# Optimization experiments

Hardware: AMD Instinct MI355X
Metric: run time of the kernel (lower is better)

## Reference

```python
import jax, jax.numpy as jnp
import numpy as np

N_NODES = 100000
N_EDGES = 3200000
B = 64            # number of graphs / RNA batch
DIM = 16          # GINE hidden dim
NFP = 33          # protein node feature dim
EMB = 128         # embedding dim
MAXLEN = 3000     # rna_global length (conv1d in_channels)
LOCLEN = 2998     # rna_local length = 3000 - log4(64) + 1
NF = 32           # n_filters
KS = 8            # conv kernel size -> 128-8+1 = 121
FC_IN = NF * 121  # 3872
BN_EPS = 1e-5


def setup_inputs() -> dict:
    key = jax.random.key(0)
    ks = jax.random.split(key, 32)
    s = 0.1
    p = {}
    # forward data args
    p['pro_x'] = jax.random.normal(ks[0], (N_NODES, NFP), jnp.float32)
    p['pro_edge_index'] = jax.random.randint(ks[1], (2, N_EDGES), 0, N_NODES, jnp.int32)
    p['pro_weight'] = jax.random.uniform(ks[2], (N_EDGES, 1), jnp.float32)
    p['pro_batch'] = jnp.sort(jax.random.randint(ks[3], (N_NODES,), 0, B, jnp.int32))
    p['rna_global'] = jax.random.randint(ks[4], (B, MAXLEN), 0, 5, jnp.int32)
    p['rna_local'] = jax.random.randint(ks[5], (B, LOCLEN), 0, 65, jnp.int32)
    # GINE layer 1 (33 -> 16)
    p['g1_w1'] = jax.random.normal(ks[6], (NFP, DIM), jnp.float32) * s
    p['g1_b1'] = jnp.zeros((DIM,), jnp.float32)
    p['g1_w2'] = jax.random.normal(ks[7], (DIM, DIM), jnp.float32) * s
    p['g1_b2'] = jnp.zeros((DIM,), jnp.float32)
    p['g1_ew'] = jax.random.normal(ks[8], (1, NFP), jnp.float32) * s  # edge Linear(1, 33)
    p['g1_eb'] = jnp.zeros((NFP,), jnp.float32)
    p['g1_eps'] = jnp.zeros((), jnp.float32)
    # GINE layers 2-5 (16 -> 16), stacked on leading axis
    p['g_w1'] = jax.random.normal(ks[9], (4, DIM, DIM), jnp.float32) * s
    p['g_b1'] = jnp.zeros((4, DIM), jnp.float32)
    p['g_w2'] = jax.random.normal(ks[10], (4, DIM, DIM), jnp.float32) * s
    p['g_b2'] = jnp.zeros((4, DIM), jnp.float32)
    p['g_ew'] = jax.random.normal(ks[11], (4, 1, DIM), jnp.float32) * s  # edge Linear(1, 16)
    p['g_eb'] = jnp.zeros((4, DIM), jnp.float32)
    p['g_eps'] = jnp.zeros((4,), jnp.float32)
    # BatchNorm1d x5
    p['bn_gamma'] = jnp.ones((5, DIM), jnp.float32)
    p['bn_beta'] = jnp.zeros((5, DIM), jnp.float32)
    # fc1_xp (16 -> 128)
    p['fc1_xp_w'] = jax.random.normal(ks[12], (DIM, EMB), jnp.float32) * s
    p['fc1_xp_b'] = jnp.zeros((EMB,), jnp.float32)
    # RNA branch
    p['emb1'] = jax.random.normal(ks[13], (5, EMB), jnp.float32)
    p['emb2'] = jax.random.normal(ks[14], (65, EMB), jnp.float32)
    p['convr1_w'] = jax.random.normal(ks[15], (NF, MAXLEN, KS), jnp.float32) * 0.01
    p['convr1_b'] = jnp.zeros((NF,), jnp.float32)
    p['convr2_w'] = jax.random.normal(ks[16], (NF, LOCLEN, KS), jnp.float32) * 0.01
    p['convr2_b'] = jnp.zeros((NF,), jnp.float32)
    p['fcxr_w'] = jax.random.normal(ks[17], (FC_IN, EMB), jnp.float32) * 0.01
    p['fcxr_b'] = jnp.zeros((EMB,), jnp.float32)
    return p


def _gine(x, src, dst, ew, w1, b1, w2, b2, ew_w, ew_b, eps):
    # GINEConv: out = MLP((1+eps)*x + sum_j relu(x_j + edge_lin(e_ij)))
    e = ew @ ew_w + ew_b                       # [E, d]
    m = jax.nn.relu(x[src] + e)                # [E, d] gather + fuse
    agg = jax.ops.segment_sum(m, dst, num_segments=N_NODES)
    h = (1.0 + eps) * x + agg
    return jax.nn.relu(h @ w1 + b1) @ w2 + b2


def _bn(x, gamma, beta):
    mu = jnp.mean(x, axis=0)
    var = jnp.var(x, axis=0)
    return (x - mu) * jax.lax.rsqrt(var + BN_EPS) * gamma + beta


def _rna_branch(tokens, emb, cw, cb, fcw, fcb):
    x = emb[tokens]                            # [B, L, 128]
    y = jax.lax.conv_general_dilated(x, cw, (1,), 'VALID',
                                     dimension_numbers=('NCH', 'OIH', 'NCH'))
    y = y + cb[None, :, None]                  # [B, 32, 121]
    return y.reshape(y.shape[0], -1) @ fcw + fcb


def reference(pro_x, pro_edge_index, pro_weight, pro_batch, rna_global, rna_local,
              g1_w1, g1_b1, g1_w2, g1_b2, g1_ew, g1_eb, g1_eps,
              g_w1, g_b1, g_w2, g_b2, g_ew, g_eb, g_eps,
              bn_gamma, bn_beta, fc1_xp_w, fc1_xp_b,
              emb1, emb2, convr1_w, convr1_b, convr2_w, convr2_b, fcxr_w, fcxr_b):
    src, dst = pro_edge_index[0], pro_edge_index[1]
    # RNA global / local branches (shared fc_xr)
    xrg = _rna_branch(rna_global, emb1, convr1_w, convr1_b, fcxr_w, fcxr_b)
    xrl = _rna_branch(rna_local, emb2, convr2_w, convr2_b, fcxr_w, fcxr_b)
    # protein GINE stack
    xp = jax.nn.relu(_gine(pro_x, src, dst, pro_weight,
                           g1_w1, g1_b1, g1_w2, g1_b2, g1_ew, g1_eb, g1_eps))
    xp = _bn(xp, bn_gamma[0], bn_beta[0])
    for i in range(4):
        xp = jax.nn.relu(_gine(xp, src, dst, pro_weight,
                               g_w1[i], g_b1[i], g_w2[i], g_b2[i],
                               g_ew[i], g_eb[i], g_eps[i]))
        xp = _bn(xp, bn_gamma[i + 1], bn_beta[i + 1])
    # global mean pool over graphs
    sums = jax.ops.segment_sum(xp, pro_batch, num_segments=B)
    cnt = jax.ops.segment_sum(jnp.ones((N_NODES, 1), xp.dtype), pro_batch, num_segments=B)
    xp = jax.nn.relu((sums / jnp.maximum(cnt, 1.0)) @ fc1_xp_w + fc1_xp_b)
    # dropout in eval mode -> identity
    xc_rna = 0.5 * (xrg + xrl)
    return (xc_rna, xp)
```

## Files before the change

### kernel.cpp

```cpp
#include <hip/hip_runtime.h>
#include <hip/hip_fp16.h>

#define N_NODES 100000
#define N_EDGES 3200000
#define BGR 64
#define DIM 16
#define NFP 33
#define ROW1 32
#define H1STR 36
#define EMB 128
#define MAXLEN 3000
#define LOCLEN 2998
#define NF 32
#define KS 8
#define OUTT 121
#define FC_IN 3872
#define BN_EPSV 1e-5f
#define POOL_CHUNK 256
#define POOL_BLKS 391
#define MLPB 391
#define AGGB1 6250
#define AGGB16 3125
#define NBIN 391
#define BCNT_BLK 512
#define P1_CHUNK 4096
#define P1_BLOCKS 782
#define MAXBIN 9088
#define NKC 32
#define KCH 121
#define WDEC (1.f / 32767.f)
#define SEG_G 8

__global__ void __launch_bounds__(256) k_bincnt(const int* __restrict__ dst,
                                                int* __restrict__ bh) {
    __shared__ int hist[NBIN];
    int t = threadIdx.x, bid = blockIdx.x;
    for (int b = t; b < NBIN; b += 256) hist[b] = 0;
    __syncthreads();
    int e0 = bid * (N_EDGES / BCNT_BLK);
    int e1 = e0 + (N_EDGES / BCNT_BLK);
    for (int e = e0 + t; e < e1; e += 256) atomicAdd(&hist[dst[e] >> 8], 1);
    __syncthreads();
    for (int b = t; b < NBIN; b += 256) bh[b * BCNT_BLK + bid] = hist[b];
}

__global__ void __launch_bounds__(512) k_binscan(const int* __restrict__ bh,
                                                 int* __restrict__ binoff,
                                                 int* __restrict__ bincur) {
    __shared__ int sc[512];
    int t = threadIdx.x;
    int s = 0;
    if (t < NBIN) {
        const int4* row = (const int4*)(bh + t * BCNT_BLK);
        #pragma unroll 4
        for (int k = 0; k < BCNT_BLK / 4; k++) {
            int4 v = row[k];
            s += v.x + v.y + v.z + v.w;
        }
    }
    sc[t] = s;
    __syncthreads();
    for (int off = 1; off < 512; off <<= 1) {
        int v = (t >= off) ? sc[t - off] : 0;
        __syncthreads();
        sc[t] += v;
        __syncthreads();
    }
    int excl = sc[t] - s;
    if (t <= NBIN) binoff[t] = excl;
    if (t < NBIN) bincur[t] = excl;
}

__global__ void __launch_bounds__(256) k_part1(const int* __restrict__ src,
                                               const int* __restrict__ dst,
                                               const float* __restrict__ w,
                                               int* __restrict__ bincur,
                                               int2* __restrict__ tmp_sw) {
    __shared__ int2 srec[P1_CHUNK];
    __shared__ unsigned short sbin[P1_CHUNK];
    __shared__ unsigned short sperm[P1_CHUNK];
    __shared__ int hist[NBIN];
    __shared__ int off[NBIN];
    __shared__ int cur[NBIN];
    __shared__ int base[NBIN];
    __shared__ int sc[512];
    int t = threadIdx.x;
    int g0 = blockIdx.x * P1_CHUNK;
    int cn = N_EDGES - g0; if (cn > P1_CHUNK) cn = P1_CHUNK;
    for (int b = t; b < NBIN; b += 256) hist[b] = 0;
    __syncthreads();
    for (int j = t; j < cn; j += 256) {
        int d = dst[g0 + j];
        int b = d >> 8;
        sbin[j] = (unsigned short)b;
        srec[j] = make_int2(src[g0 + j] | ((d & 255) << 20), __float_as_int(w[g0 + j]));
        atomicAdd(&hist[b], 1);
    }
    __syncthreads();
    sc[t] = (t < NBIN) ? hist[t] : 0;
    sc[256 + t] = (256 + t < NBIN) ? hist[256 + t] : 0;
    __syncthreads();
    for (int o = 1; o <= 256; o <<= 1) {
        int v0 = (t >= o) ? sc[t - o] : 0;
        int v1 = sc[256 + t - o];
        __syncthreads();
        sc[t] += v0;
        sc[256 + t] += v1;
        __syncthreads();
    }
    for (int b = t; b < NBIN; b += 256) {
        int e = sc[b] - hist[b];
        off[b] = e;
        cur[b] = e;
        int c = hist[b];
        base[b] = c ? atomicAdd(&bincur[b], c) : 0;
    }
    __syncthreads();
    for (int j = t; j < cn; j += 256) {
        int p = atomicAdd(&cur[sbin[j]], 1);
        sperm[p] = (unsigned short)j;
    }
    __syncthreads();
    for (int p = t; p < cn; p += 256) {
        int j = sperm[p];
        int b = sbin[j];
        tmp_sw[base[b] + (p - off[b])] = srec[j];
    }
}

__global__ void __launch_bounds__(256) k_part2(const int2* __restrict__ tmp_sw,
                                               const int* __restrict__ binoff,
                                               unsigned* __restrict__ er,
                                               int* __restrict__ ptr) {
    __shared__ unsigned char sdl[MAXBIN];
    __shared__ unsigned short perm[MAXBIN];
    __shared__ int hist[256];
    __shared__ int cur[256];
    __shared__ int sc[256];
    int t = threadIdx.x, b = blockIdx.x;
    int nlo = b << 8;
    int e0 = binoff[b], e1 = binoff[b + 1];
    int cnt = e1 - e0;
    int stage = cnt < MAXBIN ? cnt : MAXBIN;
    hist[t] = 0;
    __syncthreads();
    for (int j = t; j < stage; j += 256) {
        unsigned char dl = (unsigned char)((tmp_sw[e0 + j].x >> 20) & 255);
        sdl[j] = dl;
        atomicAdd(&hist[dl], 1);
    }
    for (int j = stage + t; j < cnt; j += 256)
        atomicAdd(&hist[(tmp_sw[e0 + j].x >> 20) & 255], 1);
    __syncthreads();
    int v = hist[t];
    sc[t] = v;
    __syncthreads();
    for (int off = 1; off < 256; off <<= 1) {
        int u = (t >= off) ? sc[t - off] : 0;
        __syncthreads();
        sc[t] += u;
        __syncthreads();
    }
    int excl = sc[t] - v;
    cur[t] = excl;
    if (nlo + t < N_NODES) ptr[nlo + t] = e0 + excl;
    if (b == NBIN - 1 && t == 0) ptr[N_NODES] = N_EDGES;
    __syncthreads();
    for (int j = t; j < stage; j += 256) {
        int p = atomicAdd(&cur[sdl[j]], 1);
        perm[p] = (unsigned short)j;
    }
    __syncthreads();
    for (int j = stage + t; j < cnt; j += 256) {
        int2 sw = tmp_sw[e0 + j];
        int p = atomicAdd(&cur[(sw.x >> 20) & 255], 1);
        unsigned wq = (unsigned)(__int_as_float(sw.y) * 32767.f + 0.5f);
        er[e0 + p] = ((unsigned)sw.x & 0x1FFFFu) | (wq << 17);
    }
    for (int p = t; p < stage; p += 256) {
        int2 sw = tmp_sw[e0 + perm[p]];
        unsigned wq = (unsigned)(__int_as_float(sw.y) * 32767.f + 0.5f);
        er[e0 + p] = ((unsigned)sw.x & 0x1FFFFu) | (wq << 17);
    }
}

__global__ void k_half1(const float* __restrict__ x, __half* __restrict__ xh,
                        __half* __restrict__ xh32) {
    int i = blockIdx.x * blockDim.x + threadIdx.x;
    if (i < N_NODES * NFP) {
        int n = i / NFP, f = i - n * NFP;
        __half v = __float2half(x[i]);
        if (f < 32) xh[n * ROW1 + f] = v;
        else xh32[n] = v;
    }
}

__global__ void __launch_bounds__(256) k_cwt(const float* __restrict__ cw,
                                             float* __restrict__ cwT, int L) {
    int l = blockIdx.x;
    int ok = threadIdx.x;
    cwT[l * 256 + ok] = cw[(ok >> 3) * (L * KS) + l * KS + (ok & 7)];
}

__device__ __forceinline__ void acc8p(float a[8], uint4 r, float wv,
                                      const float* __restrict__ ewf,
                                      const float* __restrict__ ebf) {
    float2 f01 = __half22float2(*(__half2*)&r.x);
    float2 f23 = __half22float2(*(__half2*)&r.y);
    float2 f45 = __half22float2(*(__half2*)&r.z);
    float2 f67 = __half22float2(*(__half2*)&r.w);
    float x[8] = {f01.x, f01.y, f23.x, f23.y, f45.x, f45.y, f67.x, f67.y};
    #pragma unroll
    for (int j = 0; j < 8; j++)
        a[j] += fmaxf(x[j] + fmaf(wv, ewf[j], ebf[j]), 0.f);
}

__device__ __forceinline__ void acc8s(float a[8], uint4 r, float wv,
                                      const float* __restrict__ scf,
                                      const float* __restrict__ cbf,
                                      const float* __restrict__ ewf) {
    float2 f01 = __half22float2(*(__half2*)&r.x);
    float2 f23 = __half22float2(*(__half2*)&r.y);
    float2 f45 = __half22float2(*(__half2*)&r.z);
    float2 f67 = __half22float2(*(__half2*)&r.w);
    float x[8] = {f01.x, f01.y, f23.x, f23.y, f45.x, f45.y, f67.x, f67.y};
    #pragma unroll
    for (int j = 0; j < 8; j++)
        a[j] += fmaxf(fmaf(x[j], scf[j], fmaf(wv, ewf[j], cbf[j])), 0.f);
}

__global__ void __launch_bounds__(256) k_agg1(
    const __half* __restrict__ xh, const __half* __restrict__ xh32,
    const int* __restrict__ ptr, const unsigned* __restrict__ er,
    const float* __restrict__ ew, const float* __restrict__ ebv,
    const float* __restrict__ epsp, float* __restrict__ h) {
    int t = threadIdx.x;
    int wave = t >> 6, lane = t & 63;
    int nl = lane >> 4;
    int slot = (lane >> 2) & 3;
    int q = lane & 3;
    float ewf[8], ebf[8];
    #pragma unroll
    for (int j = 0; j < 8; j++) { ewf[j] = ew[q * 8 + j]; ebf[j] = ebv[q * 8 + j]; }
    float ew32 = ew[32], eb32 = ebv[32];
    float ep = 1.f + epsp[0];
    int node = blockIdx.x * 16 + wave * 4 + nl;
    int e0 = ptr[node], e1 = ptr[node + 1];
    float a[8] = {0, 0, 0, 0, 0, 0, 0, 0};
    float a32 = 0.f;
    int i = e0 + slot;
    while (i + 4 < e1) {
        unsigned ev0 = er[i];
        unsigned ev1 = er[i + 4];
        int s0 = ev0 & 0x1FFFF, s1 = ev1 & 0x1FFFF;
        float wv0 = (float)(ev0 >> 17) * WDEC;
        float wv1 = (float)(ev1 >> 17) * WDEC;
        uint4 r0 = *(const uint4*)(xh + s0 * ROW1 + q * 8);
        uint4 r1 = *(const uint4*)(xh + s1 * ROW1 + q * 8);
        acc8p(a, r0, wv0, ewf, ebf);
        acc8p(a, r1, wv1, ewf, ebf);
        if (q == 0) {
            a32 += fmaxf(__half2float(xh32[s0]) + fmaf(wv0, ew32, eb32), 0.f);
            a32 += fmaxf(__half2float(xh32[s1]) + fmaf(wv1, ew32, eb32), 0.f);
        }
        i += 8;
    }
    if (i < e1) {
        unsigned ev = er[i];
        int s = ev & 0x1FFFF;
        float wv = (float)(ev >> 17) * WDEC;
        uint4 r = *(const uint4*)(xh + s * ROW1 + q * 8);
        acc8p(a, r, wv, ewf, ebf);
        if (q == 0)
            a32 += fmaxf(__half2float(xh32[s]) + fmaf(wv, ew32, eb32), 0.f);
    }
    #pragma unroll
    for (int j = 0; j < 8; j++) {
        a[j] += __shfl_xor(a[j], 4);
        a[j] += __shfl_xor(a[j], 8);
    }
    a32 += __shfl_xor(a32, 4);
    a32 += __shfl_xor(a32, 8);
    if (slot == 0) {
        uint4 sraw = *(const uint4*)(xh + node * ROW1 + q * 8);
        float2 s01 = __half22float2(*(__half2*)&sraw.x);
        float2 s23 = __half22float2(*(__half2*)&sraw.y);
        float2 s45 = __half22float2(*(__half2*)&sraw.z);
        float2 s67 = __half22float2(*(__half2*)&sraw.w);
        float* hp = h + node * H1STR + q * 8;
        *(float4*)hp = make_float4(ep * s01.x + a[0], ep * s01.y + a[1],
                                   ep * s23.x + a[2], ep * s23.y + a[3]);
        *(float4*)(hp + 4) = make_float4(ep * s45.x + a[4], ep * s45.y + a[5],
                                         ep * s67.x + a[6], ep * s67.y + a[7]);
        if (q == 0)
            h[node * H1STR + 32] = ep * __half2float(xh32[node]) + a32;
    }
}

__global__ void __launch_bounds__(256) k_agg16(
    const __half* __restrict__ zh, const int* __restrict__ ptr,
    const unsigned* __restrict__ er,
    const float* __restrict__ ew, const float* __restrict__ ebv,
    const float* __restrict__ epsp,
    const float* __restrict__ bnstat, const float* __restrict__ gamma,
    const float* __restrict__ beta, float* __restrict__ h) {
    int t = threadIdx.x;
    int wave = t >> 6, lane = t & 63;
    int nl = lane >> 3;
    int slot = (lane >> 1) & 3;
    int hh = lane & 1;
    float ep = 1.f + epsp[0];
    const float invn = 1.f / (float)N_NODES;
    float scf[8], shf[8], cbf[8], ewf[8];
    #pragma unroll
    for (int j = 0; j < 8; j++) {
        int f = hh * 8 + j;
        float mu = bnstat[f] * invn;
        float var = bnstat[DIM + f] * invn - mu * mu;
        float sc = gamma[f] * rsqrtf(var + BN_EPSV);
        scf[j] = sc;
        shf[j] = beta[f] - mu * sc;
        cbf[j] = shf[j] + ebv[f];
        ewf[j] = ew[f];
    }
    int node = blockIdx.x * 32 + wave * 8 + nl;
    int e0 = ptr[node], e1 = ptr[node + 1];
    float a[8] = {0, 0, 0, 0, 0, 0, 0, 0};
    int i = e0 + slot;
    while (i + 4 < e1) {
        unsigned ev0 = er[i];
        unsigned ev1 = er[i + 4];
        float wv0 = (float)(ev0 >> 17) * WDEC;
        float wv1 = (float)(ev1 >> 17) * WDEC;
        uint4 r0 = *(const uint4*)(zh + (ev0 & 0x1FFFFu) * DIM + hh * 8);
        uint4 r1 = *(const uint4*)(zh + (ev1 & 0x1FFFFu) * DIM + hh * 8);
        acc8s(a, r0, wv0, scf, cbf, ewf);
        acc8s(a, r1, wv1, scf, cbf, ewf);
        i += 8;
    }
    if (i < e1) {
        unsigned ev = er[i];
        float wv = (float)(ev >> 17) * WDEC;
        uint4 r = *(const uint4*)(zh + (ev & 0x1FFFFu) * DIM + hh * 8);
        acc8s(a, r, wv, scf, cbf, ewf);
    }
    #pragma unroll
    for (int j = 0; j < 8; j++) a[j] += __shfl_xor(a[j], 2);
    #pragma unroll
    for (int j = 0; j < 8; j++) a[j] += __shfl_xor(a[j], 4);
    if (slot == 0) {
        uint4 sraw = *(const uint4*)(zh + node * DIM + hh * 8);
        float2 s01 = __half22float2(*(__half2*)&sraw.x);
        float2 s23 = __half22float2(*(__half2*)&sraw.y);
        float2 s45 = __half22float2(*(__half2*)&sraw.z);
        float2 s67 = __half22float2(*(__half2*)&sraw.w);
        float xs[8] = {s01.x, s01.y, s23.x, s23.y, s45.x, s45.y, s67.x, s67.y};
        float o8[8];
        #pragma unroll
        for (int j = 0; j < 8; j++)
            o8[j] = ep * fmaf(xs[j], scf[j], shf[j]) + a[j];
        float* hp = h + node * DIM + hh * 8;
        *(float4*)hp = make_float4(o8[0], o8[1], o8[2], o8[3]);
        *(float4*)(hp + 4) = make_float4(o8[4], o8[5], o8[6], o8[7]);
    }
}

__device__ __forceinline__ void mlp_bn_tail(float zv[16], bool active, int t,
                                            float* __restrict__ part) {
    __shared__ float red[4][32];
    float zs[16], zq[16];
    #pragma unroll
    for (int o = 0; o < 16; o++) {
        zs[o] = active ? zv[o] : 0.f;
        zq[o] = active ? zv[o] * zv[o] : 0.f;
    }
    #pragma unroll
    for (int m = 1; m <= 32; m <<= 1) {
        #pragma unroll
        for (int o = 0; o < 16; o++) {
            zs[o] += __shfl_xor(zs[o], m);
            zq[o] += __shfl_xor(zq[o], m);
        }
    }
    int wave = t >> 6, lane = t & 63;
    if (lane == 0) {
        #pragma unroll
        for (int o = 0; o < 16; o++) {
            red[wave][o] = zs[o];
            red[wave][16 + o] = zq[o];
        }
    }
    __syncthreads();
    if (t < 32)
        part[blockIdx.x * 32 + t] = red[0][t] + red[1][t] + red[2][t] + red[3][t];
}

__device__ __forceinline__ void store_zh(__half* __restrict__ zh, int n, float zv[16]) {
    __half2 p[8];
    #pragma unroll
    for (int j = 0; j < 8; j++) p[j] = __floats2half2_rn(zv[2 * j], zv[2 * j + 1]);
    *(uint4*)(zh + n * DIM) = *(uint4*)&p[0];
    *(uint4*)(zh + n * DIM + 8) = *(uint4*)&p[4];
}

__global__ void __launch_bounds__(256) k_mlp16(
    const float* __restrict__ h,
    const float* __restrict__ W1, const float* __restrict__ b1,
    const float* __restrict__ W2, const float* __restrict__ b2,
    __half* __restrict__ zh, float* __restrict__ part) {
    __shared__ float W1s[256], W2s[256], b1s[16], b2s[16];
    int t = threadIdx.x;
    W1s[t] = W1[t];
    W2s[t] = W2[t];
    if (t < 16) { b1s[t] = b1[t]; b2s[t] = b2[t]; }
    __syncthreads();
    int n = blockIdx.x * 256 + t;
    bool active = n < N_NODES;
    float zv[16];
    if (active) {
        float hv[16];
        #pragma unroll
        for (int j = 0; j < 4; j++) {
            float4 v = *(const float4*)(h + n * DIM + j * 4);
            hv[j * 4] = v.x; hv[j * 4 + 1] = v.y; hv[j * 4 + 2] = v.z; hv[j * 4 + 3] = v.w;
        }
        float tv[16];
        #pragma unroll
        for (int o = 0; o < 16; o++) {
            float s = b1s[o];
            #pragma unroll
            for (int f = 0; f < 16; f++) s += hv[f] * W1s[f * 16 + o];
            tv[o] = fmaxf(s, 0.f);
        }
        #pragma unroll
        for (int o = 0; o < 16; o++) {
            float s = b2s[o];
            #pragma unroll
            for (int f = 0; f < 16; f++) s += tv[f] * W2s[f * 16 + o];
            zv[o] = fmaxf(s, 0.f);
        }
        store_zh(zh, n, zv);
    }
    mlp_bn_tail(zv, active, t, part);
}

__global__ void __launch_bounds__(256) k_mlp1(
    const float* __restrict__ h,
    const float* __restrict__ W1, const float* __restrict__ b1,
    const float* __restrict__ W2, const float* __restrict__ b2,
    __half* __restrict__ zh, float* __restrict__ part) {
    __shared__ float W1s[NFP * 16], W2s[256], b1s[16], b2s[16];
    int t = threadIdx.x;
    for (int j = t; j < NFP * 16; j += 256) W1s[j] = W1[j];
    W2s[t] = W2[t];
    if (t < 16) { b1s[t] = b1[t]; b2s[t] = b2[t]; }
    __syncthreads();
    int n = blockIdx.x * 256 + t;
    bool active = n < N_NODES;
    float zv[16];
    if (active) {
        float hv[NFP];
        #pragma unroll
        for (int j = 0; j < 8; j++) {
            float4 v = *(const float4*)(h + n * H1STR + j * 4);
            hv[j * 4] = v.x; hv[j * 4 + 1] = v.y; hv[j * 4 + 2] = v.z; hv[j * 4 + 3] = v.w;
        }
        hv[32] = h[n * H1STR + 32];
        float tv[16];
        #pragma unroll
        for (int o = 0; o < 16; o++) {
            float s = b1s[o];
            #pragma unroll
            for (int f = 0; f < NFP; f++) s += hv[f] * W1s[f * 16 + o];
            tv[o] = fmaxf(s, 0.f);
        }
        #pragma unroll
        for (int o = 0; o < 16; o++) {
            float s = b2s[o];
            #pragma unroll
            for (int f = 0; f < 16; f++) s += tv[f] * W2s[f * 16 + o];
            zv[o] = fmaxf(s, 0.f);
        }
        store_zh(zh, n, zv);
    }
    mlp_bn_tail(zv, active, t, part);
}

__global__ void __launch_bounds__(1024) k_bnred(const float* __restrict__ part,
                                                float* __restrict__ bnstat) {
    __shared__ float red[1024];
    int t = threadIdx.x;
    int f = t & 31, g = t >> 5;
    float s = 0.f;
    for (int i = g; i < MLPB; i += 32) s += part[i * 32 + f];
    red[t] = s;
    __syncthreads();
    for (int off = 512; off >= 32; off >>= 1) {
        if (t < off) red[t] += red[t + off];
        __syncthreads();
    }
    if (t < 32) bnstat[t] = red[t];
}

__global__ void __launch_bounds__(256) k_pool(const __half* __restrict__ zh,
                                              const int* __restrict__ batch,
                                              const float* __restrict__ bnstat,
                                              const float* __restrict__ gamma,
                                              const float* __restrict__ beta,
                                              float* __restrict__ gsum,
                                              float* __restrict__ gcnt) {
    __shared__ float lsum[BGR * DIM];
    __shared__ float lcnt[BGR];
    int t = threadIdx.x;
    for (int j = t; j < BGR * DIM; j += 256) lsum[j] = 0.f;
    if (t < BGR) lcnt[t] = 0.f;
    __syncthreads();
    int f = t & 15, r = t >> 4;
    const float invn = 1.f / (float)N_NODES;
    float mu = bnstat[f] * invn;
    float var = bnstat[DIM + f] * invn - mu * mu;
    float sc = gamma[f] * rsqrtf(var + BN_EPSV);
    float sh = beta[f] - mu * sc;
    int start = blockIdx.x * POOL_CHUNK;
    float acc = 0.f, cacc = 0.f;
    int cur = -1;
    for (int i = 0; i < POOL_CHUNK / 16; i++) {
        int n = start + r + i * 16;
        if (n >= N_NODES) break;
        int b = batch[n];
        if (b != cur) {
            if (cur >= 0) {
                atomicAdd(&lsum[cur * DIM + f], acc);
                if (f == 0) atomicAdd(&lcnt[cur], cacc);
            }
            cur = b; acc = 0.f; cacc = 0.f;
        }
        acc += fmaf(__half2float(zh[n * DIM + f]), sc, sh);
        cacc += 1.f;
    }
    if (cur >= 0) {
        atomicAdd(&lsum[cur * DIM + f], acc);
        if (f == 0) atomicAdd(&lcnt[cur], cacc);
    }
    __syncthreads();
    for (int j = t; j < BGR * DIM; j += 256) {
        float v = lsum[j];
        if (v != 0.f) atomicAdd(&gsum[j], v);
    }
    if (t < BGR) {
        float v = lcnt[t];
        if (v != 0.f) atomicAdd(&gcnt[t], v);
    }
}

__global__ void k_xp(const float* __restrict__ gsum, const float* __restrict__ gcnt,
                     const float* __restrict__ w, const float* __restrict__ bias,
                     float* __restrict__ out) {
    int b = blockIdx.x;
    int e = threadIdx.x;
    float inv = 1.f / fmaxf(gcnt[b], 1.f);
    float acc = bias[e];
    #pragma unroll
    for (int f = 0; f < DIM; f++) acc += gsum[b * DIM + f] * inv * w[f * EMB + e];
    out[b * EMB + e] = fmaxf(acc, 0.f);
}

__global__ void __launch_bounds__(256) k_bucket(const int* __restrict__ tok, int L, int V,
                                                int* __restrict__ blist,
                                                int* __restrict__ bptr) {
    __shared__ int hist[65];
    __shared__ int cursor[65];
    int b = blockIdx.x, t = threadIdx.x;
    if (t < V) hist[t] = 0;
    __syncthreads();
    for (int l = t; l < L; l += 256) atomicAdd(&hist[tok[b * L + l]], 1);
    __syncthreads();
    if (t == 0) {
        int run = 0;
        for (int v = 0; v < V; v++) {
            cursor[v] = run;
            bptr[b * (V + 1) + v] = run;
            run += hist[v];
        }
        bptr[b * (V + 1) + V] = run;
    }
    __syncthreads();
    for (int l = t; l < L; l += 256) {
        int v = tok[b * L + l];
        int p = atomicAdd(&cursor[v], 1);
        blist[b * L + p] = l;
    }
}

__global__ void __launch_bounds__(256) k_wsum_g(const int* __restrict__ blist,
                                                const int* __restrict__ bptr,
                                                const float* __restrict__ cwT,
                                                float* __restrict__ Wp) {
    int b = blockIdx.x, v = blockIdx.y, seg = blockIdx.z;
    int t = threadIdx.x;
    int s = bptr[b * 6 + v], e = bptr[b * 6 + v + 1];
    int cnt = e - s;
    int chunk = (cnt + SEG_G - 1) / SEG_G;
    int j0 = s + seg * chunk;
    int j1 = j0 + chunk; if (j1 > e) j1 = e;
    const int* bl = blist + b * MAXLEN;
    float acc = 0.f;
    int j = j0;
    while (j + 3 < j1) {
        int t0 = bl[j], t1 = bl[j + 1], t2 = bl[j + 2], t3 = bl[j + 3];
        float a0 = cwT[t0 * 256 + t];
        float a1 = cwT[t1 * 256 + t];
        float a2 = cwT[t2 * 256 + t];
        float a3 = cwT[t3 * 256 + t];
        acc += a0 + a1 + a2 + a3;
        j += 4;
    }
    while (j < j1) {
        acc += cwT[bl[j] * 256 + t];
        j++;
    }
    Wp[((b * 5 + v) * SEG_G + seg) * 256 + t] = acc;
}

__global__ void __launch_bounds__(256) k_wsum_l(const int* __restrict__ blist,
                                                const int* __restrict__ bptr,
                                                const float* __restrict__ cwT,
                                                float* __restrict__ W) {
    int b = blockIdx.x, v = blockIdx.y;
    int t = threadIdx.x;
    int s = bptr[b * 66 + v], e = bptr[b * 66 + v + 1];
    const int* bl = blist + b * LOCLEN;
    float acc = 0.f;
    int j = s;
    while (j + 3 < e) {
        int t0 = bl[j], t1 = bl[j + 1], t2 = bl[j + 2], t3 = bl[j + 3];
        float a0 = cwT[t0 * 256 + t];
        float a1 = cwT[t1 * 256 + t];
        float a2 = cwT[t2 * 256 + t];
        float a3 = cwT[t3 * 256 + t];
        acc += a0 + a1 + a2 + a3;
        j += 4;
    }
    while (j < e) {
        acc += cwT[bl[j] * 256 + t];
        j++;
    }
    int o = t >> 3, k = t & 7;
    W[((b * NF + o) * 65 + v) * KS + k] = acc;
}

__global__ void k_y(const float* __restrict__ Wpg, const float* __restrict__ Wl,
                    const float* __restrict__ emb1, const float* __restrict__ emb2,
                    const float* __restrict__ cb1, const float* __restrict__ cb2,
                    float* __restrict__ yg, float* __restrict__ yl) {
    int which = blockIdx.y;
    int bo = blockIdx.x;
    int b = bo >> 5, o = bo & 31;
    int t = threadIdx.x;
    const float* emb = which ? emb2 : emb1;
    const float* cb = which ? cb2 : cb1;
    float* y = which ? yl : yg;
    int V = which ? 65 : 5;
    __shared__ float Wsh[65 * KS];
    if (which) {
        const float* Wrow = Wl + (b * NF + o) * 65 * KS;
        for (int j = t; j < 65 * KS; j += 128) Wsh[j] = Wrow[j];
    } else {
        for (int j = t; j < 5 * KS; j += 128) {
            int v = j >> 3, k = j & 7;
            const float* p = Wpg + (b * 5 + v) * SEG_G * 256 + o * 8 + k;
            float s = 0.f;
            #pragma unroll
            for (int g = 0; g < SEG_G; g++) s += p[g * 256];
            Wsh[j] = s;
        }
    }
    __syncthreads();
    if (t < OUTT) {
        float acc = cb[o];
        for (int v = 0; v < V; v++) {
            const float* ep = emb + v * EMB + t;
            #pragma unroll
            for (int k = 0; k < KS; k++) acc += Wsh[v * KS + k] * ep[k];
        }
        y[(b * NF + o) * OUTT + t] = acc;
    }
}

__global__ void __launch_bounds__(128) k_fcpart(const float* __restrict__ yg,
                                                const float* __restrict__ yl,
                                                const float* __restrict__ w,
                                                float* __restrict__ partial) {
    int b = blockIdx.x, which = blockIdx.y, kc = blockIdx.z;
    const float* y = which ? yl : yg;
    int e = threadIdx.x;
    __shared__ float ych[KCH];
    int j0 = kc * KCH;
    if (e < KCH) ych[e] = y[b * FC_IN + j0 + e];
    __syncthreads();
    float acc = 0.f;
    #pragma unroll 4
    for (int jj = 0; jj < KCH; jj++) acc += ych[jj] * w[(j0 + jj) * EMB + e];
    partial[((which * BGR + b) * NKC + kc) * EMB + e] = acc;
}

__global__ void k_fcred(const float* __restrict__ partial, const float* __restrict__ bias,
                        float* __restrict__ out) {
    int b = blockIdx.x;
    int e = threadIdx.x;
    const float* pg = partial + b * NKC * EMB + e;
    const float* pl = partial + (BGR + b) * NKC * EMB + e;
    float ag = bias[e], al = bias[e];
    #pragma unroll
    for (int k = 0; k < NKC; k++) { ag += pg[k * EMB]; al += pl[k * EMB]; }
    out[b * EMB + e] = 0.5f * (ag + al);
}

extern "C" void kernel_launch(void* const* d_in, const int* in_sizes, int n_in,
                              void* d_out, int out_size, void* d_ws, size_t ws_size,
                              hipStream_t stream) {
    const float* pro_x = (const float*)d_in[0];
    const int* eidx = (const int*)d_in[1];
    const int* esrc = eidx;
    const int* edst = eidx + N_EDGES;
    const float* pw = (const float*)d_in[2];
    const int* batch = (const int*)d_in[3];
    const int* rg = (const int*)d_in[4];
    const int* rl = (const int*)d_in[5];
    const float* g1_w1 = (const float*)d_in[6];
    const float* g1_b1 = (const float*)d_in[7];
    const float* g1_w2 = (const float*)d_in[8];
    const float* g1_b2 = (const float*)d_in[9];
    const float* g1_ew = (const float*)d_in[10];
    const float* g1_eb = (const float*)d_in[11];
    const float* g1_eps = (const float*)d_in[12];
    const float* g_w1 = (const float*)d_in[13];
    const float* g_b1 = (const float*)d_in[14];
    const float* g_w2 = (const float*)d_in[15];
    const float* g_b2 = (const float*)d_in[16];
    const float* g_ew = (const float*)d_in[17];
    const float* g_eb = (const float*)d_in[18];
    const float* g_eps = (const float*)d_in[19];
    const float* bn_gamma = (const float*)d_in[20];
    const float* bn_beta = (const float*)d_in[21];
    const float* fc1_xp_w = (const float*)d_in[22];
    const float* fc1_xp_b = (const float*)d_in[23];
    const float* emb1 = (const float*)d_in[24];
    const float* emb2 = (const float*)d_in[25];
    const float* convr1_w = (const float*)d_in[26];
    const float* convr1_b = (const float*)d_in[27];
    const float* convr2_w = (const float*)d_in[28];
    const float* convr2_b = (const float*)d_in[29];
    const float* fcxr_w = (const float*)d_in[30];
    const float* fcxr_b = (const float*)d_in[31];
    float* out = (float*)d_out;

    float* wsf = (float*)d_ws;
    int* ptr       = (int*)wsf;        wsf += 100128;
    int* binoff    = (int*)wsf;        wsf += 512;
    int* bincur    = (int*)wsf;        wsf += 512;
    unsigned* er   = (unsigned*)wsf;   wsf += 2 * N_EDGES;
    float* stats   = wsf;              wsf += 1280;
    float* un = wsf;
    int2* tmp_sw = (int2*)un;
    int* bh      = (int*)(un + 7200000);
    float* cwTg  = un;
    float* cwTl  = un + 768000;
    __half* zh   = (__half*)(un + 1600000);
    __half* xh1  = (__half*)(un + 2400000);
    __half* xh32 = (__half*)(un + 4000000);
    float* bpart = un + 4100000;
    float* Wpg   = un + 4300000;
    float* Wl    = un + 5000000;
    float* yg    = un + 6100000;
    float* yl    = un + 6350000;
    int* blg     = (int*)(un + 6600000);
    int* bll     = (int*)(un + 6800000);
    int* bpg     = (int*)(un + 7000000);
    int* bpl     = (int*)(un + 7001000);
    float* fcpart = un + 7100000;
    float* h      = un + 7400000;
    float* gsum   = stats;
    float* gcnt   = stats + 1024;
    float* bnstat = stats + 1088;

    hipMemsetAsync(stats, 0, 1280 * sizeof(float), stream);

    k_bincnt<<<BCNT_BLK, 256, 0, stream>>>(edst, bh);
    k_binscan<<<1, 512, 0, stream>>>(bh, binoff, bincur);
    k_part1<<<P1_BLOCKS, 256, 0, stream>>>(esrc, edst, pw, bincur, tmp_sw);
    k_part2<<<NBIN, 256, 0, stream>>>(tmp_sw, binoff, er, ptr);

    k_cwt<<<MAXLEN, 256, 0, stream>>>(convr1_w, cwTg, MAXLEN);
    k_cwt<<<LOCLEN, 256, 0, stream>>>(convr2_w, cwTl, LOCLEN);

    k_half1<<<(N_NODES * NFP + 255) / 256, 256, 0, stream>>>(pro_x, xh1, xh32);

    k_bucket<<<BGR, 256, 0, stream>>>(rg, MAXLEN, 5, blg, bpg);
    k_bucket<<<BGR, 256, 0, stream>>>(rl, LOCLEN, 65, bll, bpl);
    k_wsum_g<<<dim3(BGR, 5, SEG_G), 256, 0, stream>>>(blg, bpg, cwTg, Wpg);
    k_wsum_l<<<dim3(BGR, 65), 256, 0, stream>>>(bll, bpl, cwTl, Wl);
    k_y<<<dim3(BGR * NF, 2), 128, 0, stream>>>(Wpg, Wl, emb1, emb2, convr1_b, convr2_b, yg, yl);
    k_fcpart<<<dim3(BGR, 2, NKC), 128, 0, stream>>>(yg, yl, fcxr_w, fcpart);
    k_fcred<<<BGR, 128, 0, stream>>>(fcpart, fcxr_b, out);

    k_agg1<<<AGGB1, 256, 0, stream>>>(xh1, xh32, ptr, er, g1_ew, g1_eb, g1_eps, h);
    k_mlp1<<<MLPB, 256, 0, stream>>>(h, g1_w1, g1_b1, g1_w2, g1_b2, zh, bpart);
    k_bnred<<<1, 1024, 0, stream>>>(bpart, bnstat);
    for (int i = 0; i < 4; i++) {
        k_agg16<<<AGGB16, 256, 0, stream>>>(zh, ptr, er,
                                            g_ew + i * DIM, g_eb + i * DIM, g_eps + i,
                                            bnstat + i * 32, bn_gamma + i * DIM,
                                            bn_beta + i * DIM, h);
        k_mlp16<<<MLPB, 256, 0, stream>>>(h, g_w1 + i * DIM * DIM, g_b1 + i * DIM,
                                          g_w2 + i * DIM * DIM, g_b2 + i * DIM, zh, bpart);
        k_bnred<<<1, 1024, 0, stream>>>(bpart, bnstat + (i + 1) * 32);
    }
    k_pool<<<POOL_BLKS, 256, 0, stream>>>(zh, batch, bnstat + 4 * 32,
                                          bn_gamma + 4 * DIM, bn_beta + 4 * DIM, gsum, gcnt);
    k_xp<<<BGR, EMB, 0, stream>>>(gsum, gcnt, fc1_xp_w, fc1_xp_b, out + BGR * EMB);
}
```

Measured before the change: 618.2 us.

## Merge small RNA-branch kernels and replace BN partial reduction with atomics

The paired global/local RNA kernels (weight transpose, bucketing, weighted sums) are merged into single launches indexed by block coordinate. The conv output kernel is fused with the fc partial product, so per-filter outputs stay in shared memory instead of round-tripping through global buffers. The separate one-block BatchNorm statistic reduction kernels are removed: each MLP block atomically adds its partial sums into the stats buffer, which is zeroed at the start. This cuts around a dozen launches and some global traffic, at the cost of nondeterministic float atomic summation order.

```diff
diff --git a/kernel.cpp b/kernel.cpp
--- a/kernel.cpp
+++ b/kernel.cpp
@@ -195,11 +195,18 @@
     }
 }
 
-__global__ void __launch_bounds__(256) k_cwt(const float* __restrict__ cw,
-                                             float* __restrict__ cwT, int L) {
+__global__ void __launch_bounds__(256) k_cwt2(const float* __restrict__ cw1,
+                                              const float* __restrict__ cw2,
+                                              float* __restrict__ cwTg,
+                                              float* __restrict__ cwTl) {
     int l = blockIdx.x;
     int ok = threadIdx.x;
-    cwT[l * 256 + ok] = cw[(ok >> 3) * (L * KS) + l * KS + (ok & 7)];
+    if (l < MAXLEN) {
+        cwTg[l * 256 + ok] = cw1[(ok >> 3) * (MAXLEN * KS) + l * KS + (ok & 7)];
+    } else {
+        int ll = l - MAXLEN;
+        cwTl[ll * 256 + ok] = cw2[(ok >> 3) * (LOCLEN * KS) + ll * KS + (ok & 7)];
+    }
 }
 
 __device__ __forceinline__ void acc8p(float a[8], uint4 r, float wv,
@@ -366,7 +373,7 @@
 }
 
 __device__ __forceinline__ void mlp_bn_tail(float zv[16], bool active, int t,
-                                            float* __restrict__ part) {
+                                            float* __restrict__ bnstat) {
     __shared__ float red[4][32];
     float zs[16], zq[16];
     #pragma unroll
@@ -392,7 +399,7 @@
     }
     __syncthreads();
     if (t < 32)
-        part[blockIdx.x * 32 + t] = red[0][t] + red[1][t] + red[2][t] + red[3][t];
+        atomicAdd(&bnstat[t], red[0][t] + red[1][t] + red[2][t] + red[3][t]);
 }
 
 __device__ __forceinline__ void store_zh(__half* __restrict__ zh, int n, float zv[16]) {
@@ -407,7 +414,7 @@
     const float* __restrict__ h,
     const float* __restrict__ W1, const float* __restrict__ b1,
     const float* __restrict__ W2, const float* __restrict__ b2,
-    __half* __restrict__ zh, float* __restrict__ part) {
+    __half* __restrict__ zh, float* __restrict__ bnstat) {
     __shared__ float W1s[256], W2s[256], b1s[16], b2s[16];
     int t = threadIdx.x;
     W1s[t] = W1[t];
@@ -441,14 +448,14 @@
         }
         store_zh(zh, n, zv);
     }
-    mlp_bn_tail(zv, active, t, part);
+    mlp_bn_tail(zv, active, t, bnstat);
 }
 
 __global__ void __launch_bounds__(256) k_mlp1(
     const float* __restrict__ h,
     const float* __restrict__ W1, const float* __restrict__ b1,
     const float* __restrict__ W2, const float* __restrict__ b2,
-    __half* __restrict__ zh, float* __restrict__ part) {
+    __half* __restrict__ zh, float* __restrict__ bnstat) {
     __shared__ float W1s[NFP * 16], W2s[256], b1s[16], b2s[16];
     int t = threadIdx.x;
     for (int j = t; j < NFP * 16; j += 256) W1s[j] = W1[j];
@@ -483,23 +490,7 @@
         }
         store_zh(zh, n, zv);
     }
-    mlp_bn_tail(zv, active, t, part);
-}
-
-__global__ void __launch_bounds__(1024) k_bnred(const float* __restrict__ part,
-                                                float* __restrict__ bnstat) {
-    __shared__ float red[1024];
-    int t = threadIdx.x;
-    int f = t & 31, g = t >> 5;
-    float s = 0.f;
-    for (int i = g; i < MLPB; i += 32) s += part[i * 32 + f];
-    red[t] = s;
-    __syncthreads();
-    for (int off = 512; off >= 32; off >>= 1) {
-        if (t < off) red[t] += red[t + off];
-        __syncthreads();
-    }
-    if (t < 32) bnstat[t] = red[t];
+    mlp_bn_tail(zv, active, t, bnstat);
 }
 
 __global__ void __launch_bounds__(256) k_pool(const __half* __restrict__ zh,
@@ -565,11 +556,18 @@
     out[b * EMB + e] = fmaxf(acc, 0.f);
 }
 
-__global__ void __launch_bounds__(256) k_bucket(const int* __restrict__ tok, int L, int V,
-                                                int* __restrict__ blist,
-                                                int* __restrict__ bptr) {
+__global__ void __launch_bounds__(256) k_bucket2(const int* __restrict__ tg,
+                                                 const int* __restrict__ tl,
+                                                 int* __restrict__ blg, int* __restrict__ bpg,
+                                                 int* __restrict__ bll, int* __restrict__ bpl) {
     __shared__ int hist[65];
     __shared__ int cursor[65];
+    int which = blockIdx.y;
+    const int* tok = which ? tl : tg;
+    int L = which ? LOCLEN : MAXLEN;
+    int V = which ? 65 : 5;
+    int* blist = which ? bll : blg;
+    int* bptr = which ? bpl : bpg;
     int b = blockIdx.x, t = threadIdx.x;
     if (t < V) hist[t] = 0;
     __syncthreads();
@@ -592,76 +590,81 @@
     }
 }
 
-__global__ void __launch_bounds__(256) k_wsum_g(const int* __restrict__ blist,
-                                                const int* __restrict__ bptr,
-                                                const float* __restrict__ cwT,
-                                                float* __restrict__ Wp) {
-    int b = blockIdx.x, v = blockIdx.y, seg = blockIdx.z;
+__global__ void __launch_bounds__(256) k_wsum(const int* __restrict__ blg,
+                                              const int* __restrict__ bpg,
+                                              const int* __restrict__ bll,
+                                              const int* __restrict__ bpl,
+                                              const float* __restrict__ cwTg,
+                                              const float* __restrict__ cwTl,
+                                              float* __restrict__ Wp,
+                                              float* __restrict__ Wlocal) {
+    int b = blockIdx.x, y = blockIdx.y;
     int t = threadIdx.x;
-    int s = bptr[b * 6 + v], e = bptr[b * 6 + v + 1];
-    int cnt = e - s;
-    int chunk = (cnt + SEG_G - 1) / SEG_G;
-    int j0 = s + seg * chunk;
-    int j1 = j0 + chunk; if (j1 > e) j1 = e;
-    const int* bl = blist + b * MAXLEN;
-    float acc = 0.f;
-    int j = j0;
-    while (j + 3 < j1) {
-        int t0 = bl[j], t1 = bl[j + 1], t2 = bl[j + 2], t3 = bl[j + 3];
-        float a0 = cwT[t0 * 256 + t];
-        float a1 = cwT[t1 * 256 + t];
-        float a2 = cwT[t2 * 256 + t];
-        float a3 = cwT[t3 * 256 + t];
-        acc += a0 + a1 + a2 + a3;
-        j += 4;
-    }
-    while (j < j1) {
-        acc += cwT[bl[j] * 256 + t];
-        j++;
-    }
-    Wp[((b * 5 + v) * SEG_G + seg) * 256 + t] = acc;
-}
-
-__global__ void __launch_bounds__(256) k_wsum_l(const int* __restrict__ blist,
-                                                const int* __restrict__ bptr,
-                                                const float* __restrict__ cwT,
-                                                float* __restrict__ W) {
-    int b = blockIdx.x, v = blockIdx.y;
-    int t = threadIdx.x;
-    int s = bptr[b * 66 + v], e = bptr[b * 66 + v + 1];
-    const int* bl = blist + b * LOCLEN;
-    float acc = 0.f;
-    int j = s;
-    while (j + 3 < e) {
-        int t0 = bl[j], t1 = bl[j + 1], t2 = bl[j + 2], t3 = bl[j + 3];
-        float a0 = cwT[t0 * 256 + t];
-        float a1 = cwT[t1 * 256 + t];
-        float a2 = cwT[t2 * 256 + t];
-        float a3 = cwT[t3 * 256 + t];
-        acc += a0 + a1 + a2 + a3;
-        j += 4;
-    }
-    while (j < e) {
-        acc += cwT[bl[j] * 256 + t];
-        j++;
-    }
-    int o = t >> 3, k = t & 7;
-    W[((b * NF + o) * 65 + v) * KS + k] = acc;
-}
-
-__global__ void k_y(const float* __restrict__ Wpg, const float* __restrict__ Wl,
-                    const float* __restrict__ emb1, const float* __restrict__ emb2,
-                    const float* __restrict__ cb1, const float* __restrict__ cb2,
-                    float* __restrict__ yg, float* __restrict__ yl) {
+    if (y < 40) {
+        int v = y >> 3, seg = y & 7;
+        int s = bpg[b * 6 + v], e = bpg[b * 6 + v + 1];
+        int cnt = e - s;
+        int chunk = (cnt + SEG_G - 1) / SEG_G;
+        int j0 = s + seg * chunk;
+        int j1 = j0 + chunk; if (j1 > e) j1 = e;
+        const int* bl = blg + b * MAXLEN;
+        float acc = 0.f;
+        int j = j0;
+        while (j + 3 < j1) {
+            int t0 = bl[j], t1 = bl[j + 1], t2 = bl[j + 2], t3 = bl[j + 3];
+            float a0 = cwTg[t0 * 256 + t];
+            float a1 = cwTg[t1 * 256 + t];
+            float a2 = cwTg[t2 * 256 + t];
+            float a3 = cwTg[t3 * 256 + t];
+            acc += a0 + a1 + a2 + a3;
+            j += 4;
+        }
+        while (j < j1) {
+            acc += cwTg[bl[j] * 256 + t];
+            j++;
+        }
+        Wp[((b * 5 + v) * SEG_G + seg) * 256 + t] = acc;
+    } else {
+        int v = y - 40;
+        int s = bpl[b * 66 + v], e = bpl[b * 66 + v + 1];
+        const int* bl = bll + b * LOCLEN;
+        float acc = 0.f;
+        int j = s;
+        while (j + 3 < e) {
+            int t0 = bl[j], t1 = bl[j + 1], t2 = bl[j + 2], t3 = bl[j + 3];
+            float a0 = cwTl[t0 * 256 + t];
+            float a1 = cwTl[t1 * 256 + t];
+            float a2 = cwTl[t2 * 256 + t];
+            float a3 = cwTl[t3 * 256 + t];
+            acc += a0 + a1 + a2 + a3;
+            j += 4;
+        }
+        while (j < e) {
+            acc += cwTl[bl[j] * 256 + t];
+            j++;
+        }
+        int o = t >> 3, k = t & 7;
+        Wlocal[((b * NF + o) * 65 + v) * KS + k] = acc;
+    }
+}
+
+__global__ void __launch_bounds__(128) k_yfc(const float* __restrict__ Wpg,
+                                             const float* __restrict__ Wl,
+                                             const float* __restrict__ emb1,
+                                             const float* __restrict__ emb2,
+                                             const float* __restrict__ cb1,
+                                             const float* __restrict__ cb2,
+                                             const float* __restrict__ w,
+                                             float* __restrict__ partial) {
     int which = blockIdx.y;
     int bo = blockIdx.x;
     int b = bo >> 5, o = bo & 31;
     int t = threadIdx.x;
     const float* emb = which ? emb2 : emb1;
     const float* cb = which ? cb2 : cb1;
-    float* y = which ? yl : yg;
     int V = which ? 65 : 5;
     __shared__ float Wsh[65 * KS];
+    __shared__ float ych[OUTT];
     if (which) {
         const float* Wrow = Wl + (b * NF + o) * 65 * KS;
         for (int j = t; j < 65 * KS; j += 128) Wsh[j] = Wrow[j];
@@ -683,25 +686,14 @@
             #pragma unroll
             for (int k = 0; k < KS; k++) acc += Wsh[v * KS + k] * ep[k];
         }
-        y[(b * NF + o) * OUTT + t] = acc;
-    }
-}
-
-__global__ void __launch_bounds__(128) k_fcpart(const float* __restrict__ yg,
-                                                const float* __restrict__ yl,
-                                                const float* __restrict__ w,
-                                                float* __restrict__ partial) {
-    int b = blockIdx.x, which = blockIdx.y, kc = blockIdx.z;
-    const float* y = which ? yl : yg;
-    int e = threadIdx.x;
-    __shared__ float ych[KCH];
-    int j0 = kc * KCH;
-    if (e < KCH) ych[e] = y[b * FC_IN + j0 + e];
-    __syncthreads();
-    float acc = 0.f;
+        ych[t] = acc;
+    }
+    __syncthreads();
+    float facc = 0.f;
+    const float* wp = w + (o * OUTT) * EMB + t;
     #pragma unroll 4
-    for (int jj = 0; jj < KCH; jj++) acc += ych[jj] * w[(j0 + jj) * EMB + e];
-    partial[((which * BGR + b) * NKC + kc) * EMB + e] = acc;
+    for (int jj = 0; jj < OUTT; jj++) facc += ych[jj] * wp[jj * EMB];
+    partial[((which * BGR + b) * NKC + o) * EMB + t] = facc;
 }
 
 __global__ void k_fcred(const float* __restrict__ partial, const float* __restrict__ bias,
@@ -769,11 +761,8 @@
     __half* zh   = (__half*)(un + 1600000);
     __half* xh1  = (__half*)(un + 2400000);
     __half* xh32 = (__half*)(un + 4000000);
-    float* bpart = un + 4100000;
     float* Wpg   = un + 4300000;
     float* Wl    = un + 5000000;
-    float* yg    = un + 6100000;
-    float* yl    = un + 6350000;
     int* blg     = (int*)(un + 6600000);
     int* bll     = (int*)(un + 6800000);
     int* bpg     = (int*)(un + 7000000);
@@ -791,30 +780,26 @@
     k_part1<<<P1_BLOCKS, 256, 0, stream>>>(esrc, edst, pw, bincur, tmp_sw);
     k_part2<<<NBIN, 256, 0, stream>>>(tmp_sw, binoff, er, ptr);
 
-    k_cwt<<<MAXLEN, 256, 0, stream>>>(convr1_w, cwTg, MAXLEN);
-    k_cwt<<<LOCLEN, 256, 0, stream>>>(convr2_w, cwTl, LOCLEN);
+    k_cwt2<<<MAXLEN + LOCLEN, 256, 0, stream>>>(convr1_w, convr2_w, cwTg, cwTl);
 
     k_half1<<<(N_NODES * NFP + 255) / 256, 256, 0, stream>>>(pro_x, xh1, xh32);
 
-    k_bucket<<<BGR, 256, 0, stream>>>(rg, MAXLEN, 5, blg, bpg);
-    k_bucket<<<BGR, 256, 0, stream>>>(rl, LOCLEN, 65, bll, bpl);
-    k_wsum_g<<<dim3(BGR, 5, SEG_G), 256, 0, stream>>>(blg, bpg, cwTg, Wpg);
-    k_wsum_l<<<dim3(BGR, 65), 256, 0, stream>>>(bll, bpl, cwTl, Wl);
-    k_y<<<dim3(BGR * NF, 2), 128, 0, stream>>>(Wpg, Wl, emb1, emb2, convr1_b, convr2_b, yg, yl);
-    k_fcpart<<<dim3(BGR, 2, NKC), 128, 0, stream>>>(yg, yl, fcxr_w, fcpart);
+    k_bucket2<<<dim3(BGR, 2), 256, 0, stream>>>(rg, rl, blg, bpg, bll, bpl);
+    k_wsum<<<dim3(BGR, 105), 256, 0, stream>>>(blg, bpg, bll, bpl, cwTg, cwTl, Wpg, Wl);
+    k_yfc<<<dim3(BGR * NF, 2), 128, 0, stream>>>(Wpg, Wl, emb1, emb2, convr1_b, convr2_b,
+                                                 fcxr_w, fcpart);
     k_fcred<<<BGR, 128, 0, stream>>>(fcpart, fcxr_b, out);
 
     k_agg1<<<AGGB1, 256, 0, stream>>>(xh1, xh32, ptr, er, g1_ew, g1_eb, g1_eps, h);
-    k_mlp1<<<MLPB, 256, 0, stream>>>(h, g1_w1, g1_b1, g1_w2, g1_b2, zh, bpart);
-    k_bnred<<<1, 1024, 0, stream>>>(bpart, bnstat);
+    k_mlp1<<<MLPB, 256, 0, stream>>>(h, g1_w1, g1_b1, g1_w2, g1_b2, zh, bnstat);
     for (int i = 0; i < 4; i++) {
         k_agg16<<<AGGB16, 256, 0, stream>>>(zh, ptr, er,
                                             g_ew + i * DIM, g_eb + i * DIM, g_eps + i,
                                             bnstat + i * 32, bn_gamma + i * DIM,
                                             bn_beta + i * DIM, h);
         k_mlp16<<<MLPB, 256, 0, stream>>>(h, g_w1 + i * DIM * DIM, g_b1 + i * DIM,
-                                          g_w2 + i * DIM * DIM, g_b2 + i * DIM, zh, bpart);
-        k_bnred<<<1, 1024, 0, stream>>>(bpart, bnstat + (i + 1) * 32);
+                                          g_w2 + i * DIM * DIM, g_b2 + i * DIM, zh,
+                                          bnstat + (i + 1) * 32);
     }
     k_pool<<<POOL_BLKS, 256, 0, stream>>>(zh, batch, bnstat + 4 * 32,
                                           bn_gamma + 4 * DIM, bn_beta + 4 * DIM, gsum, gcnt);
```

Measured after the change: 571.5 us. 1.08x faster.
